# Performance work log

Hardware: AMD Instinct MI355X
Metric: run time of the kernel (lower is better)

Reference implementation:

```python
import jax, jax.numpy as jnp
import numpy as np
import math

EMBED_DIM = 512
NUM_HEADS = 8
BLOCK_SIZE = 16
RANK = 32
B, N = 1, 4096
HEAD_DIM = EMBED_DIM // NUM_HEADS
SCALE = math.sqrt(HEAD_DIM)  # note: the torch module MULTIPLIES q by sqrt(head_dim)


def _block_causal_mask(n, block):
    # block-diagonal lower-triangular mask, identical for every head
    idx = jnp.arange(n)
    same_block = (idx[:, None] // block) == (idx[None, :] // block)
    causal = idx[:, None] >= idx[None, :]
    return (same_block & causal).astype(jnp.float32)  # [N, N]


def setup_inputs() -> dict:
    key = jax.random.key(0)
    ks = jax.random.split(key, 12)
    s = 0.02
    C, R = EMBED_DIM, RANK
    return {
        "x": jax.random.normal(ks[0], (B, N, C), dtype=jnp.float32),
        # low-rank query proj: Linear(C->R) then Linear(R->C); torch weight is [out, in]
        "q_w1": jax.random.normal(ks[1], (R, C), dtype=jnp.float32) * s,
        "q_w2": jax.random.normal(ks[2], (C, R), dtype=jnp.float32) * s,
        # key_value: Linear(C->2R) then Linear(2R->2C)
        "kv_w1": jax.random.normal(ks[3], (2 * R, C), dtype=jnp.float32) * s,
        "kv_w2": jax.random.normal(ks[4], (2 * C, 2 * R), dtype=jnp.float32) * s,
        # dynamic_focus: depthwise 1x1 conv (per-channel scale+bias) then pointwise 1x1 conv
        "dw_w": jax.random.normal(ks[5], (C,), dtype=jnp.float32) * s,
        "dw_b": jax.random.normal(ks[6], (C,), dtype=jnp.float32) * s,
        "pw_w": jax.random.normal(ks[7], (C, C), dtype=jnp.float32) * s,
        "pw_b": jax.random.normal(ks[8], (C,), dtype=jnp.float32) * s,
        # output proj: Linear(C->R) then Linear(R->C)
        "p_w1": jax.random.normal(ks[9], (R, C), dtype=jnp.float32) * s,
        "p_w2": jax.random.normal(ks[10], (C, R), dtype=jnp.float32) * s,
    }


def reference(x, q_w1, q_w2, kv_w1, kv_w2, dw_w, dw_b, pw_w, pw_b, p_w1, p_w2):
    Bv, Nv, C = x.shape
    H, D = NUM_HEADS, HEAD_DIM

    # low-rank q / kv projections (no bias)
    q = (x @ q_w1.T) @ q_w2.T                              # [B, N, C]
    kv = (x @ kv_w1.T) @ kv_w2.T                           # [B, N, 2C]

    q = q.reshape(Bv, Nv, H, D).transpose(0, 2, 1, 3)      # [B, H, N, D]
    kv = kv.reshape(Bv, Nv, 2, H, D).transpose(2, 0, 3, 1, 4)
    k, v = kv[0], kv[1]                                    # [B, H, N, D]

    q = q * SCALE
    attn = jnp.einsum("bhnd,bhmd->bhnm", q, k)             # [B, H, N, N]
    # faithful to source: full-row softmax FIRST, then block-diag causal mask
    mask = _block_causal_mask(Nv, BLOCK_SIZE)              # [N, N]
    attn = jax.nn.softmax(attn, axis=-1) * mask

    wv = jnp.einsum("bhnm,bhmd->bhnd", attn, v)            # [B, H, N, D]
    wv = wv.transpose(0, 2, 1, 3).reshape(Bv, Nv, C)       # [B, N, C]

    # dynamic_focus: depthwise 1x1 conv == per-channel affine; pointwise 1x1 conv == linear.
    # Spatial reshape to (sqrt(N), sqrt(N)) is a no-op for 1x1 convs, so stay in [B, N, C].
    dyn = wv * dw_w + dw_b
    dyn = dyn @ pw_w.T + pw_b

    y = dyn + x
    y = (y @ p_w1.T) @ p_w2.T
    return y
```

## Files before the change

kernel.cpp:

```cpp
#include <hip/hip_runtime.h>

#define NFULL 4096
#define CDIM  512
#define HEADS 8
#define DDIM  64

typedef unsigned short u16;
typedef short bf16x8 __attribute__((ext_vector_type(8)));
typedef float f32x4 __attribute__((ext_vector_type(4)));

#if __has_builtin(__builtin_amdgcn_exp2f)
__device__ __forceinline__ float exp2_hw(float x) { return __builtin_amdgcn_exp2f(x); }
#else
__device__ __forceinline__ float exp2_hw(float x) {
  float r;
  asm volatile("v_exp_f32 %0, %1\n\ts_nop 1" : "=v"(r) : "v"(x));
  return r;
}
#endif
#define EXP2(x) exp2_hw(x)

#define QSCALE 11.541560327111707f

__device__ __forceinline__ float dot4(float4 a, float4 b) {
  return a.x * b.x + a.y * b.y + a.z * b.z + a.w * b.w;
}

__device__ __forceinline__ u16 f2bf(float x) {
  union { float f; unsigned u; } v; v.f = x;
  unsigned r = v.u + 0x7fffu + ((v.u >> 16) & 1u);
  return (u16)(r >> 16);
}

__device__ __forceinline__ float bf2f(u16 b) {
  union { unsigned u; float f; } v; v.u = ((unsigned)b) << 16;
  return v.f;
}

__global__ __launch_bounds__(256) void k_pre(const float* __restrict__ x,
                                             const float* __restrict__ qw1,
                                             const float* __restrict__ kvw1,
                                             u16* __restrict__ t_bf,
                                             const float* __restrict__ pww,
                                             const float* __restrict__ dww,
                                             const float* __restrict__ dwb,
                                             const float* __restrict__ pwb,
                                             const float* __restrict__ pw1,
                                             const float* __restrict__ pw2,
                                             float* __restrict__ bias2,
                                             u16* __restrict__ pwbf,
                                             u16* __restrict__ pw1bf,
                                             u16* __restrict__ pw2bf) {
  __shared__ __align__(16) u16 Xs[32][72];
  __shared__ __align__(16) u16 Ws[96][72];
  const int tid = threadIdx.x;

  if (blockIdx.x >= 128) {
    const int b = blockIdx.x - 128;
    if (b < 2) {
      const int c = b * 256 + tid;
      float acc = 0.f;
      for (int e = 0; e < 512; e += 4)
        acc += dot4(*(const float4*)&pww[(size_t)c * 512 + e], *(const float4*)&dwb[e]);
      bias2[c] = acc + pwb[c];
    } else {
      const float* src;
      u16* dst;
      bool scale = false;
      int base;
      if (b < 66)      { base = (b - 2) * 4096 + tid * 16;  src = pww; dst = pwbf; scale = true; }
      else if (b < 70) { base = (b - 66) * 4096 + tid * 16; src = pw1; dst = pw1bf; }
      else             { base = (b - 70) * 4096 + tid * 16; src = pw2; dst = pw2bf; }
      const int e0 = base & 511;
      u16 o[16];
#pragma unroll
      for (int q = 0; q < 4; ++q) {
        float4 w = *(const float4*)&src[base + q * 4];
        if (scale) {
          const float4 d = *(const float4*)&dww[e0 + q * 4];
          w.x *= d.x; w.y *= d.y; w.z *= d.z; w.w *= d.w;
        }
        o[q * 4 + 0] = f2bf(w.x); o[q * 4 + 1] = f2bf(w.y);
        o[q * 4 + 2] = f2bf(w.z); o[q * 4 + 3] = f2bf(w.w);
      }
      *(uint4*)&dst[base] = *(const uint4*)&o[0];
      *(uint4*)&dst[base + 8] = *(const uint4*)&o[8];
    }
    return;
  }

  const int r0 = blockIdx.x * 32;
  const int wave = tid >> 6, lane = tid & 63;
  const int lrow = lane & 15, g = lane >> 4;
  const int rs = wave >> 1, ws2 = wave & 1;

  f32x4 acc[3];
#pragma unroll
  for (int sub = 0; sub < 3; ++sub) acc[sub] = (f32x4){0.f, 0.f, 0.f, 0.f};

  for (int k0 = 0; k0 < 512; k0 += 64) {
    __syncthreads();
    {
      const int row = tid >> 3, c16 = (tid & 7) * 8;
      const float* __restrict__ src = x + (size_t)(r0 + row) * 512 + k0 + c16;
      const float4 v0 = *(const float4*)(src);
      const float4 v1 = *(const float4*)(src + 4);
      u16 tmp[8] = {f2bf(v0.x), f2bf(v0.y), f2bf(v0.z), f2bf(v0.w),
                    f2bf(v1.x), f2bf(v1.y), f2bf(v1.z), f2bf(v1.w)};
      *(uint4*)&Xs[row][c16] = *(const uint4*)&tmp[0];
    }
    for (int u = tid; u < 768; u += 256) {
      const int c = u >> 3, c16 = (u & 7) * 8;
      const float* __restrict__ src =
          (c < 32 ? qw1 + (size_t)c * 512 : kvw1 + (size_t)(c - 32) * 512) + k0 + c16;
      const float4 v0 = *(const float4*)(src);
      const float4 v1 = *(const float4*)(src + 4);
      u16 tmp[8] = {f2bf(v0.x), f2bf(v0.y), f2bf(v0.z), f2bf(v0.w),
                    f2bf(v1.x), f2bf(v1.y), f2bf(v1.z), f2bf(v1.w)};
      *(uint4*)&Ws[c][c16] = *(const uint4*)&tmp[0];
    }
    __syncthreads();
    const bf16x8 a0 = *(const bf16x8*)&Xs[rs * 16 + lrow][g * 8];
    const bf16x8 a1 = *(const bf16x8*)&Xs[rs * 16 + lrow][32 + g * 8];
#pragma unroll
    for (int sub = 0; sub < 3; ++sub) {
      const int c = (ws2 * 3 + sub) * 16 + lrow;
      const bf16x8 b0 = *(const bf16x8*)&Ws[c][g * 8];
      const bf16x8 b1 = *(const bf16x8*)&Ws[c][32 + g * 8];
      acc[sub] = __builtin_amdgcn_mfma_f32_16x16x32_bf16(a0, b0, acc[sub], 0, 0, 0);
      acc[sub] = __builtin_amdgcn_mfma_f32_16x16x32_bf16(a1, b1, acc[sub], 0, 0, 0);
    }
  }
#pragma unroll
  for (int sub = 0; sub < 3; ++sub)
#pragma unroll
    for (int j = 0; j < 4; ++j)
      t_bf[(size_t)(r0 + rs * 16 + g * 4 + j) * 96 + (ws2 * 3 + sub) * 16 + lrow] =
          f2bf(acc[sub][j]);
}

__global__ __launch_bounds__(256) void k_proj2(const u16* __restrict__ t_bf,
                                               const float* __restrict__ qw2,
                                               const float* __restrict__ kvw2,
                                               u16* __restrict__ qb,
                                               u16* __restrict__ kb,
                                               float* __restrict__ vh) {
  __shared__ __align__(16) u16 Ts[64][72];
  __shared__ __align__(16) u16 Wsh[128][72];
  const int cb = blockIdx.x % 12;
  const int r0 = (blockIdx.x / 12) * 64;
  const int tid = threadIdx.x;
  const int wave = tid >> 6, lane = tid & 63;
  const int lrow = lane & 15, g = lane >> 4;
  const bool isq = cb < 4;
  const int c0 = isq ? cb * 128 : 512 + (cb - 4) * 128;

  for (int u = tid; u < 512; u += 256) {
    const int row = u >> 3, ch = (u & 7) * 8;
    uint4 v = {0u, 0u, 0u, 0u};
    if (isq) {
      if (ch < 32) v = *(const uint4*)&t_bf[(size_t)(r0 + row) * 96 + ch];
    } else {
      v = *(const uint4*)&t_bf[(size_t)(r0 + row) * 96 + 32 + ch];
    }
    *(uint4*)&Ts[row][ch] = v;
  }
  if (isq) {
    for (int u = tid; u < 1024; u += 256) {
      const int col = u >> 3, cf = (u & 7) * 4;
      const float4 v = *(const float4*)&qw2[(size_t)(c0 + col) * 32 + cf];
      u16 tmp[4] = {f2bf(v.x), f2bf(v.y), f2bf(v.z), f2bf(v.w)};
      *(uint2*)&Wsh[col][cf] = *(const uint2*)&tmp[0];
    }
  } else {
    for (int u = tid; u < 2048; u += 256) {
      const int col = u >> 4, cf = (u & 15) * 4;
      const float4 v = *(const float4*)&kvw2[(size_t)(c0 - 512 + col) * 64 + cf];
      u16 tmp[4] = {f2bf(v.x), f2bf(v.y), f2bf(v.z), f2bf(v.w)};
      *(uint2*)&Wsh[col][cf] = *(const uint2*)&tmp[0];
    }
  }
  __syncthreads();

  if (isq) {
    const bf16x8 aq = *(const bf16x8*)&Ts[wave * 16 + lrow][g * 8];
#pragma unroll
    for (int sub = 0; sub < 8; ++sub) {
      const bf16x8 b0 = *(const bf16x8*)&Wsh[sub * 16 + lrow][g * 8];
      f32x4 acc = {0.f, 0.f, 0.f, 0.f};
      acc = __builtin_amdgcn_mfma_f32_16x16x32_bf16(aq, b0, acc, 0, 0, 0);
      const int colg = c0 + sub * 16 + lrow;
#pragma unroll
      for (int j = 0; j < 4; ++j) {
        const int n = r0 + wave * 16 + g * 4 + j;
        qb[((size_t)(colg >> 6) * NFULL + n) * 64 + (colg & 63)] = f2bf(acc[j] * QSCALE);
      }
    }
  } else {
    const bf16x8 a0 = *(const bf16x8*)&Ts[wave * 16 + lrow][g * 8];
    const bf16x8 a1 = *(const bf16x8*)&Ts[wave * 16 + lrow][32 + g * 8];
#pragma unroll
    for (int sub = 0; sub < 8; ++sub) {
      const bf16x8 b0 = *(const bf16x8*)&Wsh[sub * 16 + lrow][g * 8];
      const bf16x8 b1 = *(const bf16x8*)&Wsh[sub * 16 + lrow][32 + g * 8];
      f32x4 acc = {0.f, 0.f, 0.f, 0.f};
      acc = __builtin_amdgcn_mfma_f32_16x16x32_bf16(a0, b0, acc, 0, 0, 0);
      acc = __builtin_amdgcn_mfma_f32_16x16x32_bf16(a1, b1, acc, 0, 0, 0);
      const int colg = c0 + sub * 16 + lrow;
#pragma unroll
      for (int j = 0; j < 4; ++j) {
        const int n = r0 + wave * 16 + g * 4 + j;
        if (colg < 1024) {
          const int c2 = colg - 512;
          kb[((size_t)(c2 >> 6) * NFULL + n) * 64 + (c2 & 63)] = f2bf(acc[j]);
        } else {
          const int c2 = colg - 1024;
          vh[((size_t)(c2 >> 6) * NFULL + n) * 64 + (c2 & 63)] = acc[j];
        }
      }
    }
  }
}

__global__ __launch_bounds__(256, 4) void k_attn(const u16* __restrict__ qb,
                                                 const u16* __restrict__ kb,
                                                 const float* __restrict__ vh,
                                                 u16* __restrict__ wv16,
                                                 float* __restrict__ dsp) {
  __shared__ __align__(16) u16 KB[4][64][64];
  __shared__ float P_lds[4][16][17];
  __shared__ float Ds[4][4][16];

  const int h = blockIdx.x & 7;
  const int qt = (blockIdx.x >> 3) & 63;
  const int s = blockIdx.x >> 9;
  const int q0 = qt * 64;
  const int tid = threadIdx.x;
  const int wave = tid >> 6, lane = tid & 63;
  const int lrow = lane & 15, g = lane >> 4;

  const u16* __restrict__ Qg = qb + ((size_t)h * NFULL + q0) * 64;
  const u16* __restrict__ Kg = kb + ((size_t)h * NFULL + (size_t)s * 2048) * 64;

  bf16x8 qf[4][2];
#pragma unroll
  for (int f = 0; f < 4; ++f) {
    qf[f][0] = *(const bf16x8*)&Qg[(f * 16 + lrow) * 64 + g * 8];
    qf[f][1] = *(const bf16x8*)&Qg[(f * 16 + lrow) * 64 + 32 + g * 8];
  }

  const int srow8 = lane >> 3;
  const int scol = ((lane & 7) ^ srow8) << 3;

#define STAGE(T, B)                                                           \
  do {                                                                        \
    const u16* tb_ = Kg + (size_t)(T) * 64 * 64;                              \
    {                                                                         \
      const u16* src_ = tb_ + (wave * 16 + srow8) * 64 + scol;                \
      u16* dst_ = &KB[(B)][wave * 16][0];                                     \
      __builtin_amdgcn_global_load_lds(                                       \
          (const __attribute__((address_space(1))) unsigned*)src_,            \
          (__attribute__((address_space(3))) unsigned*)dst_, 16, 0, 0);       \
    }                                                                         \
    {                                                                         \
      const u16* src_ = tb_ + (wave * 16 + 8 + srow8) * 64 + scol;            \
      u16* dst_ = &KB[(B)][wave * 16][0] + 512;                               \
      __builtin_amdgcn_global_load_lds(                                       \
          (const __attribute__((address_space(1))) unsigned*)src_,            \
          (__attribute__((address_space(3))) unsigned*)dst_, 16, 0, 0);       \
    }                                                                         \
  } while (0)

  const int rsw = wave * 16 + lrow;
  const int x0 = (g ^ (lrow & 7)) * 8;
  const int x1 = ((g + 4) ^ (lrow & 7)) * 8;

  float dsum[4] = {0.f, 0.f, 0.f, 0.f};
  const bool dg = (s == (qt >> 5));
  const int tdiag = qt & 31;

  auto tile = [&](int t, int b) {
    const bf16x8 kf0 = *(const bf16x8*)&KB[b][rsw][x0];
    const bf16x8 kf1 = *(const bf16x8*)&KB[b][rsw][x1];
    f32x4 a[4];
    __builtin_amdgcn_s_setprio(1);
#pragma unroll
    for (int f = 0; f < 4; ++f) {
      f32x4 t4 = {0.f, 0.f, 0.f, 0.f};
      t4 = __builtin_amdgcn_mfma_f32_16x16x32_bf16(kf0, qf[f][0], t4, 0, 0, 0);
      t4 = __builtin_amdgcn_mfma_f32_16x16x32_bf16(kf1, qf[f][1], t4, 0, 0, 0);
      a[f] = t4;
    }
    __builtin_amdgcn_s_setprio(0);
    const bool isd = dg && (t == tdiag);
#pragma unroll
    for (int f = 0; f < 4; ++f) {
      const float e0 = EXP2(a[f][0]);
      const float e1 = EXP2(a[f][1]);
      const float e2 = EXP2(a[f][2]);
      const float e3 = EXP2(a[f][3]);
      dsum[f] += (e0 + e1) + (e2 + e3);
      if (isd && f == wave) {
        const int rr = g * 4;
        P_lds[wave][rr + 0][lrow] = (rr + 0 <= lrow) ? e0 : 0.f;
        P_lds[wave][rr + 1][lrow] = (rr + 1 <= lrow) ? e1 : 0.f;
        P_lds[wave][rr + 2][lrow] = (rr + 2 <= lrow) ? e2 : 0.f;
        P_lds[wave][rr + 3][lrow] = (rr + 3 <= lrow) ? e3 : 0.f;
      }
    }
  };

  STAGE(0, 0); STAGE(1, 1); STAGE(2, 2);

  for (int t = 0; t < 28; t += 2) {
    STAGE(t + 3, (t + 3) & 3);
    asm volatile("s_waitcnt vmcnt(6)" ::: "memory");
    tile(t, t & 3);
    STAGE(t + 4, (t + 4) & 3);
    asm volatile("s_waitcnt vmcnt(6)" ::: "memory");
    tile(t + 1, (t + 1) & 3);
  }
  STAGE(31, 3);
  asm volatile("s_waitcnt vmcnt(6)" ::: "memory");
  tile(28, 0);
  asm volatile("s_waitcnt vmcnt(4)" ::: "memory");
  tile(29, 1);
  asm volatile("s_waitcnt vmcnt(2)" ::: "memory");
  tile(30, 2);
  asm volatile("s_waitcnt vmcnt(0)" ::: "memory");
  tile(31, 3);
#undef STAGE

#pragma unroll
  for (int f = 0; f < 4; ++f) {
    dsum[f] += __shfl_xor(dsum[f], 16);
    dsum[f] += __shfl_xor(dsum[f], 32);
  }
  if (g == 0) {
#pragma unroll
    for (int f = 0; f < 4; ++f) Ds[wave][f][lrow] = dsum[f];
  }
  __syncthreads();

  if (tid < 64) {
    const int f = tid >> 4, r = tid & 15;
    const float den = Ds[0][f][r] + Ds[1][f][r] + Ds[2][f][r] + Ds[3][f][r];
    dsp[((size_t)s * HEADS + h) * NFULL + q0 + f * 16 + r] = den;
  }

  if (dg) {
    const float* __restrict__ V =
        vh + ((size_t)h * NFULL + q0 + wave * 16) * 64 + g * 16;
    float o[16];
#pragma unroll
    for (int dd = 0; dd < 16; ++dd) o[dd] = 0.f;
#pragma unroll
    for (int k = 0; k < 16; ++k) {
      const float p = P_lds[wave][k][lrow];
      const float4 v0 = *(const float4*)&V[k * 64 + 0];
      const float4 v1 = *(const float4*)&V[k * 64 + 4];
      const float4 v2 = *(const float4*)&V[k * 64 + 8];
      const float4 v3 = *(const float4*)&V[k * 64 + 12];
      o[0] += p * v0.x;  o[1] += p * v0.y;  o[2] += p * v0.z;  o[3] += p * v0.w;
      o[4] += p * v1.x;  o[5] += p * v1.y;  o[6] += p * v1.z;  o[7] += p * v1.w;
      o[8] += p * v2.x;  o[9] += p * v2.y;  o[10] += p * v2.z; o[11] += p * v2.w;
      o[12] += p * v3.x; o[13] += p * v3.y; o[14] += p * v3.z; o[15] += p * v3.w;
    }
    u16 ob[16];
#pragma unroll
    for (int dd = 0; dd < 16; ++dd) ob[dd] = f2bf(o[dd]);
    u16* __restrict__ op =
        wv16 + (size_t)(q0 + wave * 16 + lrow) * CDIM + h * 64 + g * 16;
    *(uint4*)&op[0] = *(const uint4*)&ob[0];
    *(uint4*)&op[8] = *(const uint4*)&ob[8];
  }
}

__global__ __launch_bounds__(256) void k_dyn(const u16* __restrict__ wv16,
                                             const float* __restrict__ x,
                                             const u16* __restrict__ pwbf,
                                             const float* __restrict__ bias2,
                                             const float* __restrict__ dsp,
                                             u16* __restrict__ y16) {
  __shared__ __align__(16) u16 Ab[64][72];
  __shared__ __align__(16) u16 Wb[64][72];
  const int rb = blockIdx.x >> 3, cb = blockIdx.x & 7;
  const int r0 = rb * 64, c0 = cb * 64;
  const int tid = threadIdx.x;
  const int wave = tid >> 6, lane = tid & 63;
  const int lrow = lane & 15, g = lane >> 4;
  const int srow = tid >> 2;
  const int skc = (tid & 3) * 16;

  float inv8[8];
#pragma unroll
  for (int hh = 0; hh < 8; ++hh) {
    const size_t base = (size_t)hh * NFULL + r0 + srow;
    inv8[hh] = 1.0f / (dsp[base] + dsp[(size_t)8 * NFULL + base]);
  }

  f32x4 acc[4];
#pragma unroll
  for (int ct = 0; ct < 4; ++ct) acc[ct] = (f32x4){0.f, 0.f, 0.f, 0.f};

  const u16* __restrict__ ap = wv16 + (size_t)(r0 + srow) * 512 + skc;
  const u16* __restrict__ wp = pwbf + (size_t)(c0 + srow) * 512 + skc;
  uint4 av0 = *(const uint4*)ap;
  uint4 av1 = *(const uint4*)(ap + 8);
  uint4 w0 = *(const uint4*)wp;
  uint4 w1 = *(const uint4*)(wp + 8);

  for (int k0 = 0; k0 < 512; k0 += 64) {
    const float sc = inv8[k0 >> 6];
    u16 ab16[16];
    const u16* pa0 = (const u16*)&av0;
    const u16* pa1 = (const u16*)&av1;
#pragma unroll
    for (int e = 0; e < 8; ++e) ab16[e] = f2bf(bf2f(pa0[e]) * sc);
#pragma unroll
    for (int e = 0; e < 8; ++e) ab16[8 + e] = f2bf(bf2f(pa1[e]) * sc);
    __syncthreads();
    *(uint4*)&Ab[srow][skc] = *(const uint4*)&ab16[0];
    *(uint4*)&Ab[srow][skc + 8] = *(const uint4*)&ab16[8];
    *(uint4*)&Wb[srow][skc] = w0;
    *(uint4*)&Wb[srow][skc + 8] = w1;
    __syncthreads();
    if (k0 + 64 < 512) {
      av0 = *(const uint4*)(ap + k0 + 64);
      av1 = *(const uint4*)(ap + k0 + 64 + 8);
      w0 = *(const uint4*)(wp + k0 + 64);
      w1 = *(const uint4*)(wp + k0 + 64 + 8);
    }
#pragma unroll
    for (int kk = 0; kk < 2; ++kk) {
      const bf16x8 af = *(const bf16x8*)&Ab[wave * 16 + lrow][kk * 32 + g * 8];
#pragma unroll
      for (int ct = 0; ct < 4; ++ct) {
        const bf16x8 wf = *(const bf16x8*)&Wb[ct * 16 + lrow][kk * 32 + g * 8];
        acc[ct] = __builtin_amdgcn_mfma_f32_16x16x32_bf16(wf, af, acc[ct], 0, 0, 0);
      }
    }
  }
  const int row = r0 + wave * 16 + lrow;
#pragma unroll
  for (int ct = 0; ct < 4; ++ct) {
    const int c = c0 + ct * 16 + g * 4;
    const float4 bb = *(const float4*)&bias2[c];
    const float4 xv = *(const float4*)&x[(size_t)row * 512 + c];
    u16 o4[4];
    o4[0] = f2bf(acc[ct][0] + bb.x + xv.x);
    o4[1] = f2bf(acc[ct][1] + bb.y + xv.y);
    o4[2] = f2bf(acc[ct][2] + bb.z + xv.z);
    o4[3] = f2bf(acc[ct][3] + bb.w + xv.w);
    *(uint2*)&y16[(size_t)row * 512 + c] = *(const uint2*)o4;
  }
}

__global__ __launch_bounds__(256) void k_pout(const u16* __restrict__ y16,
                                              const u16* __restrict__ pw1bf,
                                              const u16* __restrict__ pw2bf,
                                              float* __restrict__ out) {
  __shared__ __align__(16) u16 yb[16][520];
  __shared__ float tp_part[2][32][17];
  const int r0 = blockIdx.x * 16;
  const int tid = threadIdx.x;
  const int wave = tid >> 6, lane = tid & 63;
  const int lrow = lane & 15, g = lane >> 4;

  for (int rep = 0; rep < 4; ++rep) {
    const int idx = rep * 256 + tid;
    const int row = idx >> 6, c8 = (idx & 63) * 8;
    *(uint4*)&yb[row][c8] = *(const uint4*)&y16[(size_t)(r0 + row) * 512 + c8];
  }
  __syncthreads();

  {
    const int ct1 = wave & 1, kh = wave >> 1;
    f32x4 acc = {0.f, 0.f, 0.f, 0.f};
#pragma unroll
    for (int ks = 0; ks < 8; ++ks) {
      const int K = kh * 256 + ks * 32 + g * 8;
      const bf16x8 aw = *(const bf16x8*)&pw1bf[(size_t)(ct1 * 16 + lrow) * 512 + K];
      const bf16x8 bf = *(const bf16x8*)&yb[lrow][K];
      acc = __builtin_amdgcn_mfma_f32_16x16x32_bf16(aw, bf, acc, 0, 0, 0);
    }
#pragma unroll
    for (int j = 0; j < 4; ++j)
      tp_part[kh][ct1 * 16 + g * 4 + j][lrow] = acc[j];
  }
  __syncthreads();

  union { u16 a[8]; bf16x8 v; } bq;
#pragma unroll
  for (int i = 0; i < 8; ++i) {
    const int k = g * 8 + i;
    bq.a[i] = f2bf(tp_part[0][k][lrow] + tp_part[1][k][lrow]);
  }

#pragma unroll
  for (int t = 0; t < 8; ++t) {
    const int ct = wave * 8 + t;
    const bf16x8 aw = *(const bf16x8*)&pw2bf[(size_t)(ct * 16 + lrow) * 32 + g * 8];
    f32x4 acc = {0.f, 0.f, 0.f, 0.f};
    acc = __builtin_amdgcn_mfma_f32_16x16x32_bf16(aw, bq.v, acc, 0, 0, 0);
    float4 res;
    res.x = acc[0]; res.y = acc[1]; res.z = acc[2]; res.w = acc[3];
    *(float4*)&out[(size_t)(r0 + lrow) * 512 + ct * 16 + g * 4] = res;
  }
}

extern "C" void kernel_launch(void* const* d_in, const int* in_sizes, int n_in,
                              void* d_out, int out_size, void* d_ws, size_t ws_size,
                              hipStream_t stream) {
  const float* x     = (const float*)d_in[0];
  const float* q_w1  = (const float*)d_in[1];
  const float* q_w2  = (const float*)d_in[2];
  const float* kv_w1 = (const float*)d_in[3];
  const float* kv_w2 = (const float*)d_in[4];
  const float* dw_w  = (const float*)d_in[5];
  const float* dw_b  = (const float*)d_in[6];
  const float* pw_w  = (const float*)d_in[7];
  const float* pw_b  = (const float*)d_in[8];
  const float* p_w1  = (const float*)d_in[9];
  const float* p_w2  = (const float*)d_in[10];
  float* out = (float*)d_out;

  char* ws = (char*)d_ws;
  float* dsp   = (float*)ws;
  float* bias2 = (float*)(ws + 262144);
  u16*   pwbf  = (u16*)(ws + 262144 + 4096);
  u16*   pw1bf = pwbf + 262144;
  u16*   pw2bf = pw1bf + 16384;
  u16*   t_bf  = pw2bf + 16384;
  u16*   qbw   = t_bf + (size_t)NFULL * 96;
  u16*   kbw   = qbw + (size_t)HEADS * NFULL * DDIM;
  float* vh    = (float*)(kbw + (size_t)HEADS * NFULL * DDIM);
  u16*   wv16  = (u16*)(vh + (size_t)HEADS * NFULL * DDIM);
  u16*   y16   = qbw;

  k_pre<<<202, 256, 0, stream>>>(x, q_w1, kv_w1, t_bf, pw_w, dw_w, dw_b, pw_b,
                                 p_w1, p_w2, bias2, pwbf, pw1bf, pw2bf);
  k_proj2<<<(NFULL / 64) * 12, 256, 0, stream>>>(t_bf, q_w2, kv_w2, qbw, kbw, vh);
  k_attn<<<2 * HEADS * (NFULL / 64), 256, 0, stream>>>(qbw, kbw, vh, wv16, dsp);
  k_dyn<<<(NFULL / 64) * 8, 256, 0, stream>>>(wv16, x, pwbf, bias2, dsp, y16);
  k_pout<<<NFULL / 16, 256, 0, stream>>>(y16, pw1bf, pw2bf, out);
}
```

Before: 83.33 us.

## Split attention keys four ways, vectorize projection stores, split output projection blocks

```diff
diff --git a/kernel.cpp b/kernel.cpp
--- a/kernel.cpp
+++ b/kernel.cpp
@@ -127,16 +127,17 @@
       const int c = (ws2 * 3 + sub) * 16 + lrow;
       const bf16x8 b0 = *(const bf16x8*)&Ws[c][g * 8];
       const bf16x8 b1 = *(const bf16x8*)&Ws[c][32 + g * 8];
-      acc[sub] = __builtin_amdgcn_mfma_f32_16x16x32_bf16(a0, b0, acc[sub], 0, 0, 0);
-      acc[sub] = __builtin_amdgcn_mfma_f32_16x16x32_bf16(a1, b1, acc[sub], 0, 0, 0);
-    }
-  }
-#pragma unroll
-  for (int sub = 0; sub < 3; ++sub)
-#pragma unroll
-    for (int j = 0; j < 4; ++j)
-      t_bf[(size_t)(r0 + rs * 16 + g * 4 + j) * 96 + (ws2 * 3 + sub) * 16 + lrow] =
-          f2bf(acc[sub][j]);
+      acc[sub] = __builtin_amdgcn_mfma_f32_16x16x32_bf16(b0, a0, acc[sub], 0, 0, 0);
+      acc[sub] = __builtin_amdgcn_mfma_f32_16x16x32_bf16(b1, a1, acc[sub], 0, 0, 0);
+    }
+  }
+  const int n = r0 + rs * 16 + lrow;
+#pragma unroll
+  for (int sub = 0; sub < 3; ++sub) {
+    u16 o4[4] = {f2bf(acc[sub][0]), f2bf(acc[sub][1]),
+                 f2bf(acc[sub][2]), f2bf(acc[sub][3])};
+    *(uint2*)&t_bf[(size_t)n * 96 + (ws2 * 3 + sub) * 16 + g * 4] = *(const uint2*)o4;
+  }
 }
 
 __global__ __launch_bounds__(256) void k_proj2(const u16* __restrict__ t_bf,
@@ -182,19 +183,19 @@
   }
   __syncthreads();
 
+  const int n = r0 + wave * 16 + lrow;
   if (isq) {
     const bf16x8 aq = *(const bf16x8*)&Ts[wave * 16 + lrow][g * 8];
 #pragma unroll
     for (int sub = 0; sub < 8; ++sub) {
       const bf16x8 b0 = *(const bf16x8*)&Wsh[sub * 16 + lrow][g * 8];
       f32x4 acc = {0.f, 0.f, 0.f, 0.f};
-      acc = __builtin_amdgcn_mfma_f32_16x16x32_bf16(aq, b0, acc, 0, 0, 0);
-      const int colg = c0 + sub * 16 + lrow;
-#pragma unroll
-      for (int j = 0; j < 4; ++j) {
-        const int n = r0 + wave * 16 + g * 4 + j;
-        qb[((size_t)(colg >> 6) * NFULL + n) * 64 + (colg & 63)] = f2bf(acc[j] * QSCALE);
-      }
+      acc = __builtin_amdgcn_mfma_f32_16x16x32_bf16(b0, aq, acc, 0, 0, 0);
+      const int colg0 = c0 + sub * 16 + g * 4;
+      const int hh = colg0 >> 6, d0 = colg0 & 63;
+      u16 o4[4] = {f2bf(acc[0] * QSCALE), f2bf(acc[1] * QSCALE),
+                   f2bf(acc[2] * QSCALE), f2bf(acc[3] * QSCALE)};
+      *(uint2*)&qb[((size_t)hh * NFULL + n) * 64 + d0] = *(const uint2*)o4;
     }
   } else {
     const bf16x8 a0 = *(const bf16x8*)&Ts[wave * 16 + lrow][g * 8];
@@ -204,19 +205,20 @@
       const bf16x8 b0 = *(const bf16x8*)&Wsh[sub * 16 + lrow][g * 8];
       const bf16x8 b1 = *(const bf16x8*)&Wsh[sub * 16 + lrow][32 + g * 8];
       f32x4 acc = {0.f, 0.f, 0.f, 0.f};
-      acc = __builtin_amdgcn_mfma_f32_16x16x32_bf16(a0, b0, acc, 0, 0, 0);
-      acc = __builtin_amdgcn_mfma_f32_16x16x32_bf16(a1, b1, acc, 0, 0, 0);
-      const int colg = c0 + sub * 16 + lrow;
-#pragma unroll
-      for (int j = 0; j < 4; ++j) {
-        const int n = r0 + wave * 16 + g * 4 + j;
-        if (colg < 1024) {
-          const int c2 = colg - 512;
-          kb[((size_t)(c2 >> 6) * NFULL + n) * 64 + (c2 & 63)] = f2bf(acc[j]);
-        } else {
-          const int c2 = colg - 1024;
-          vh[((size_t)(c2 >> 6) * NFULL + n) * 64 + (c2 & 63)] = acc[j];
-        }
+      acc = __builtin_amdgcn_mfma_f32_16x16x32_bf16(b0, a0, acc, 0, 0, 0);
+      acc = __builtin_amdgcn_mfma_f32_16x16x32_bf16(b1, a1, acc, 0, 0, 0);
+      const int colg0 = c0 + sub * 16 + g * 4;
+      if (colg0 < 1024) {
+        const int c2 = colg0 - 512;
+        const int hh = c2 >> 6, d0 = c2 & 63;
+        u16 o4[4] = {f2bf(acc[0]), f2bf(acc[1]), f2bf(acc[2]), f2bf(acc[3])};
+        *(uint2*)&kb[((size_t)hh * NFULL + n) * 64 + d0] = *(const uint2*)o4;
+      } else {
+        const int c2 = colg0 - 1024;
+        const int hh = c2 >> 6, d0 = c2 & 63;
+        float4 o4;
+        o4.x = acc[0]; o4.y = acc[1]; o4.z = acc[2]; o4.w = acc[3];
+        *(float4*)&vh[((size_t)hh * NFULL + n) * 64 + d0] = o4;
       }
     }
   }
@@ -240,7 +242,7 @@
   const int lrow = lane & 15, g = lane >> 4;
 
   const u16* __restrict__ Qg = qb + ((size_t)h * NFULL + q0) * 64;
-  const u16* __restrict__ Kg = kb + ((size_t)h * NFULL + (size_t)s * 2048) * 64;
+  const u16* __restrict__ Kg = kb + ((size_t)h * NFULL + (size_t)s * 1024) * 64;
 
   bf16x8 qf[4][2];
 #pragma unroll
@@ -276,14 +278,13 @@
   const int x1 = ((g + 4) ^ (lrow & 7)) * 8;
 
   float dsum[4] = {0.f, 0.f, 0.f, 0.f};
-  const bool dg = (s == (qt >> 5));
-  const int tdiag = qt & 31;
+  const bool dg = (s == (qt >> 4));
+  const int tdiag = qt & 15;
 
   auto tile = [&](int t, int b) {
     const bf16x8 kf0 = *(const bf16x8*)&KB[b][rsw][x0];
     const bf16x8 kf1 = *(const bf16x8*)&KB[b][rsw][x1];
     f32x4 a[4];
-    __builtin_amdgcn_s_setprio(1);
 #pragma unroll
     for (int f = 0; f < 4; ++f) {
       f32x4 t4 = {0.f, 0.f, 0.f, 0.f};
@@ -291,7 +292,6 @@
       t4 = __builtin_amdgcn_mfma_f32_16x16x32_bf16(kf1, qf[f][1], t4, 0, 0, 0);
       a[f] = t4;
     }
-    __builtin_amdgcn_s_setprio(0);
     const bool isd = dg && (t == tdiag);
 #pragma unroll
     for (int f = 0; f < 4; ++f) {
@@ -312,23 +312,17 @@
 
   STAGE(0, 0); STAGE(1, 1); STAGE(2, 2);
 
-  for (int t = 0; t < 28; t += 2) {
+  for (int t = 0; t < 13; ++t) {
     STAGE(t + 3, (t + 3) & 3);
     asm volatile("s_waitcnt vmcnt(6)" ::: "memory");
     tile(t, t & 3);
-    STAGE(t + 4, (t + 4) & 3);
-    asm volatile("s_waitcnt vmcnt(6)" ::: "memory");
-    tile(t + 1, (t + 1) & 3);
-  }
-  STAGE(31, 3);
-  asm volatile("s_waitcnt vmcnt(6)" ::: "memory");
-  tile(28, 0);
+  }
   asm volatile("s_waitcnt vmcnt(4)" ::: "memory");
-  tile(29, 1);
+  tile(13, 1);
   asm volatile("s_waitcnt vmcnt(2)" ::: "memory");
-  tile(30, 2);
+  tile(14, 2);
   asm volatile("s_waitcnt vmcnt(0)" ::: "memory");
-  tile(31, 3);
+  tile(15, 3);
 #undef STAGE
 
 #pragma unroll
@@ -396,7 +390,8 @@
 #pragma unroll
   for (int hh = 0; hh < 8; ++hh) {
     const size_t base = (size_t)hh * NFULL + r0 + srow;
-    inv8[hh] = 1.0f / (dsp[base] + dsp[(size_t)8 * NFULL + base]);
+    inv8[hh] = 1.0f / (dsp[base] + dsp[(size_t)8 * NFULL + base] +
+                       dsp[(size_t)16 * NFULL + base] + dsp[(size_t)24 * NFULL + base]);
   }
 
   f32x4 acc[4];
@@ -462,7 +457,8 @@
                                               float* __restrict__ out) {
   __shared__ __align__(16) u16 yb[16][520];
   __shared__ float tp_part[2][32][17];
-  const int r0 = blockIdx.x * 16;
+  const int r0 = (blockIdx.x >> 1) * 16;
+  const int chalf = blockIdx.x & 1;
   const int tid = threadIdx.x;
   const int wave = tid >> 6, lane = tid & 63;
   const int lrow = lane & 15, g = lane >> 4;
@@ -498,8 +494,8 @@
   }
 
 #pragma unroll
-  for (int t = 0; t < 8; ++t) {
-    const int ct = wave * 8 + t;
+  for (int t = 0; t < 4; ++t) {
+    const int ct = chalf * 16 + wave * 4 + t;
     const bf16x8 aw = *(const bf16x8*)&pw2bf[(size_t)(ct * 16 + lrow) * 32 + g * 8];
     f32x4 acc = {0.f, 0.f, 0.f, 0.f};
     acc = __builtin_amdgcn_mfma_f32_16x16x32_bf16(aw, bq.v, acc, 0, 0, 0);
@@ -527,8 +523,8 @@
 
   char* ws = (char*)d_ws;
   float* dsp   = (float*)ws;
-  float* bias2 = (float*)(ws + 262144);
-  u16*   pwbf  = (u16*)(ws + 262144 + 4096);
+  float* bias2 = (float*)(ws + 524288);
+  u16*   pwbf  = (u16*)(ws + 524288 + 4096);
   u16*   pw1bf = pwbf + 262144;
   u16*   pw2bf = pw1bf + 16384;
   u16*   t_bf  = pw2bf + 16384;
@@ -541,7 +537,7 @@
   k_pre<<<202, 256, 0, stream>>>(x, q_w1, kv_w1, t_bf, pw_w, dw_w, dw_b, pw_b,
                                  p_w1, p_w2, bias2, pwbf, pw1bf, pw2bf);
   k_proj2<<<(NFULL / 64) * 12, 256, 0, stream>>>(t_bf, q_w2, kv_w2, qbw, kbw, vh);
-  k_attn<<<2 * HEADS * (NFULL / 64), 256, 0, stream>>>(qbw, kbw, vh, wv16, dsp);
+  k_attn<<<4 * HEADS * (NFULL / 64), 256, 0, stream>>>(qbw, kbw, vh, wv16, dsp);
   k_dyn<<<(NFULL / 64) * 8, 256, 0, stream>>>(wv16, x, pwbf, bias2, dsp, y16);
-  k_pout<<<NFULL / 16, 256, 0, stream>>>(y16, pw1bf, pw2bf, out);
-}
+  k_pout<<<(NFULL / 16) * 2, 256, 0, stream>>>(y16, pw1bf, pw2bf, out);
+}
```

After: 161.3 us. 1.94x slower.
